# Kernel optimization log

Hardware: AMD Instinct MI355X
Metric: run time of the kernel (lower is better)

Reference implementation:

```python
import jax, jax.numpy as jnp
import numpy as np
from jax import lax

IMG = 1280
VAR0, VAR1 = 0.1, 0.2          # SSD decode variances
CONF_T = 0.7                    # confidence threshold
NMS_T = 0.4                     # IoU threshold
K = 1000                        # fixed NMS candidate budget (jit-friendly)
MIN_SIZES = [[16, 32], [64, 128], [256, 512]]
STEPS = [8, 16, 32]


def make_priors():
    """Vectorized priorbox: [cx, cy, w, h] normalized to [0,1]. N = 67200."""
    out = []
    for ms, s in zip(MIN_SIZES, STEPS):
        f = IMG // s
        ii, jj = np.meshgrid(np.arange(f), np.arange(f), indexing='ij')
        cx = (jj + 0.5) * s / IMG
        cy = (ii + 0.5) * s / IMG
        per_m = [np.stack([cx, cy, np.full_like(cx, m / IMG, dtype=np.float64),
                           np.full_like(cx, m / IMG, dtype=np.float64)], axis=-1)
                 for m in ms]
        a = np.stack(per_m, axis=2)  # [f, f, n_min_sizes, 4] -> matches (i, j, min_size) loop order
        out.append(a.reshape(-1, 4))
    return np.concatenate(out, axis=0).astype(np.float32)


def setup_inputs() -> dict:
    key = jax.random.key(0)
    k1, k2, k3 = jax.random.split(key, 3)
    N = 67200
    loc = jax.random.normal(k1, (1, N, 4), dtype=jnp.float32)
    conf = jax.random.normal(k2, (1, N, 2), dtype=jnp.float32)
    land = jax.random.normal(k3, (1, N, 10), dtype=jnp.float32)
    priors = jnp.asarray(make_priors())
    return {"loc": loc, "conf": conf, "land": land, "priors": priors}


def _decode_boxes(loc, priors):
    # center-form decode then convert to corner form (x1,y1,x2,y2)
    xy = priors[:, :2] + loc[:, :2] * VAR0 * priors[:, 2:]
    wh = priors[:, 2:] * jnp.exp(loc[:, 2:] * VAR1)
    x1y1 = xy - wh * 0.5
    return jnp.concatenate([x1y1, x1y1 + wh], axis=-1)


def _decode_landm(land, priors):
    l = land.reshape(-1, 5, 2)  # 5 landmark points
    pts = priors[:, None, :2] + l * VAR0 * priors[:, None, 2:]
    return pts.reshape(-1, 10)


def _pairwise_iou(b):
    # b: [K, 4] corner-form
    area = (b[:, 2] - b[:, 0]) * (b[:, 3] - b[:, 1])
    lt = jnp.maximum(b[:, None, :2], b[None, :, :2])
    rb = jnp.minimum(b[:, None, 2:], b[None, :, 2:])
    wh = jnp.clip(rb - lt, 0.0)
    inter = wh[..., 0] * wh[..., 1]
    return inter / (area[:, None] + area[None, :] - inter + 1e-12)


def reference(loc, conf, land, priors):
    scores_all = jax.nn.softmax(conf[0], axis=-1)[:, 1]          # [N]
    boxes_all = _decode_boxes(loc[0], priors) * IMG              # [N, 4]
    landms_all = _decode_landm(land[0], priors) * IMG            # [N, 10]

    # threshold (torch.where) + fixed-size top-K selection for jit
    masked = jnp.where(scores_all > CONF_T, scores_all, -jnp.inf)
    top_s, idx = lax.top_k(masked, K)                            # sorted descending
    b = boxes_all[idx]
    lm = landms_all[idx]
    s = scores_all[idx]
    valid = top_s > CONF_T                                       # slots that passed threshold

    # greedy NMS over score-sorted candidates
    iou = _pairwise_iou(b)                                       # [K, K]
    ar = jnp.arange(K)

    def body(i, keep):
        sup = (iou[i] > NMS_T) & (ar > i) & keep[i]
        return keep & ~sup

    keep = lax.fori_loop(0, K, body, valid)

    boxes_out = jnp.where(keep[:, None], b, 0.0)
    scores_out = jnp.where(keep, s, 0.0)
    landms_out = jnp.where(keep[:, None], lm, 0.0)
    return boxes_out, scores_out, landms_out
```

## Files before the change

### kernel.cpp

```cpp
#include <hip/hip_runtime.h>
#include <stdint.h>

#define N_ANCH 67200
#define KCAP   1000
#define CONF_THR 0.7f
#define NMS_THR  0.4f

#define BUCK_BASE 0x3F333333u
#define BUCK_SHIFT 10
#define NBUCK 5120
#define CAPG 4096

#define MID_BLKS 32
#define SUP_BLKS 63

#define OFF_CTR   0
#define OFF_HIST  64
#define OFF_FILL  20544
#define OFF_LIST  41024
#define OFF_GKEYS 578624
#define OFF_SCORE 611392
#define OFF_BOX   615488
#define OFF_LM    631872
#define OFF_SUP   672832

__device__ inline unsigned long long shfl_xor_u64(unsigned long long v, int m) {
    unsigned int lo = (unsigned int)__shfl_xor((int)(v & 0xffffffffull), m, 64);
    unsigned int hi = (unsigned int)__shfl_xor((int)(v >> 32), m, 64);
    return ((unsigned long long)hi << 32) | lo;
}

__device__ inline int bucket_of(unsigned int sb) {
    return min((int)((sb - BUCK_BASE) >> BUCK_SHIFT), NBUCK - 1);
}

__device__ inline void findcut_and_scan(int* sufx, int* swsum, int* sB,
                                        int tid, int lane, int wv) {
    if (tid < 64) {
        int acc = 0, B = 0;
        bool found = false;
        for (int t = 0; t < NBUCK / 64 && !found; ++t) {
            int base = NBUCK - 64 * (t + 1);
            int c = sufx[base + lane];
            int ssum = c;
#pragma unroll
            for (int off = 1; off < 64; off <<= 1)
                ssum += __shfl_xor(ssum, off, 64);
            if (acc + ssum >= KCAP) {
                for (int l = 63; l >= 0; --l) {
                    int cl = (int)__builtin_amdgcn_readlane((unsigned int)c, l);
                    if (acc + cl >= KCAP) { B = base + l; found = true; break; }
                    acc += cl;
                }
            } else {
                acc += ssum;
            }
        }
        if (lane == 0) *sB = found ? B : 0;
    }
    __syncthreads();
    int c[5];
#pragma unroll
    for (int k = 0; k < 5; ++k)
        c[k] = sufx[NBUCK - 1 - (tid * 5 + k)];
    int tsum = c[0] + c[1] + c[2] + c[3] + c[4];
    int inc = tsum;
#pragma unroll
    for (int off = 1; off < 64; off <<= 1) {
        int n = __shfl_up(inc, off, 64);
        if (lane >= off) inc += n;
    }
    if (lane == 63) swsum[wv] = inc;
    __syncthreads();
    if (tid < 16) {
        int v = swsum[tid];
        int s = v;
#pragma unroll
        for (int off = 1; off < 16; off <<= 1) {
            int n = __shfl_up(s, off, 64);
            if (tid >= off) s += n;
        }
        swsum[tid] = s - v;
    }
    __syncthreads();
    int run = swsum[wv] + inc - tsum;
#pragma unroll
    for (int k = 0; k < 5; ++k) {
        sufx[NBUCK - 1 - (tid * 5 + k)] = run;
        run += c[k];
    }
    __syncthreads();
}

__global__ __launch_bounds__(1024) void k_zero(int* __restrict__ ctr,
                                               int* __restrict__ hist,
                                               int* __restrict__ gfill) {
    int tid = threadIdx.x;
    if (tid < 16) ctr[tid] = 0;
    for (int t = tid; t < NBUCK; t += 1024) { hist[t] = 0; gfill[t] = 0; }
}

__global__ __launch_bounds__(256) void k_front(const float* __restrict__ conf,
                                               unsigned long long* __restrict__ list,
                                               int* __restrict__ hist,
                                               int* __restrict__ ctr) {
    int t = blockIdx.x * 256 + threadIdx.x;
    int lane = threadIdx.x & 63;
    int a0 = t * 2;
    bool p0 = false, p1 = false;
    unsigned long long k0 = 0ull, k1 = 0ull;
    if (a0 < N_ANCH) {
        float4 c = reinterpret_cast<const float4*>(conf)[t];
        {
            float mx = fmaxf(c.x, c.y);
            float e0 = expf(c.x - mx), e1 = expf(c.y - mx);
            float s = e1 / (e0 + e1);
            if (s > CONF_THR) {
                p0 = true;
                k0 = ((unsigned long long)__float_as_uint(s) << 32)
                   | (unsigned int)(0xFFFFFFFFu - (unsigned int)a0);
            }
        }
        {
            float mx = fmaxf(c.z, c.w);
            float e0 = expf(c.z - mx), e1 = expf(c.w - mx);
            float s = e1 / (e0 + e1);
            if (s > CONF_THR) {
                p1 = true;
                k1 = ((unsigned long long)__float_as_uint(s) << 32)
                   | (unsigned int)(0xFFFFFFFFu - (unsigned int)(a0 + 1));
            }
        }
    }
    unsigned long long m0 = __ballot(p0);
    unsigned long long m1 = __ballot(p1);
    int n0 = (int)__popcll(m0), n1 = (int)__popcll(m1);
    int base = 0;
    if ((n0 + n1) > 0) {
        if (lane == 0) base = atomicAdd(&ctr[0], n0 + n1);
        base = __shfl(base, 0, 64);
        unsigned long long below = (1ull << lane) - 1ull;
        if (p0) {
            list[base + (int)__popcll(m0 & below)] = k0;
            atomicAdd(&hist[bucket_of((unsigned int)(k0 >> 32))], 1);
        }
        if (p1) {
            list[base + n0 + (int)__popcll(m1 & below)] = k1;
            atomicAdd(&hist[bucket_of((unsigned int)(k1 >> 32))], 1);
        }
    }
}

__global__ __launch_bounds__(1024) void k_midrank(
        const unsigned long long* __restrict__ list,
        const int* __restrict__ hist,
        int* __restrict__ gfill,
        unsigned long long* __restrict__ gkeys,
        int* __restrict__ ctr,
        const float* __restrict__ loc,
        const float* __restrict__ land,
        const float* __restrict__ priors,
        float* __restrict__ sel_score,
        float* __restrict__ sel_box,
        float* __restrict__ sel_lm) {
#pragma clang fp contract(off)
    __shared__ int sufx[NBUCK];
    __shared__ int swsum[16];
    __shared__ int sB;
    __shared__ int slast;
    int tid = threadIdx.x, lane = tid & 63, wv = tid >> 6;
    for (int t = tid; t < NBUCK; t += 1024) sufx[t] = hist[t];
    __syncthreads();
    findcut_and_scan(sufx, swsum, &sB, tid, lane, wv);
    int B = sB;
    int M = min(ctr[0], N_ANCH);

    for (int p = blockIdx.x * 1024 + tid; p < M; p += MID_BLKS * 1024) {
        unsigned long long k = list[p];
        int b = bucket_of((unsigned int)(k >> 32));
        if (b >= B) {
            int off = atomicAdd(&gfill[b], 1);
            int slot = sufx[b] + off;
            if (slot < CAPG) gkeys[slot] = k;
        }
    }
    __syncthreads();
    if (tid == 0) {
        __threadfence();
        int old = atomicAdd(&ctr[1], 1);
        slast = (old == MID_BLKS - 1);
    }
    __syncthreads();
    if (!slast) return;
    if (tid == 0) __threadfence();
    __syncthreads();

    int S = min((B > 0) ? sufx[B - 1] : M, CAPG);
    for (int s = tid; s < S; s += 1024) {
        unsigned long long key = gkeys[s];
        unsigned int sb = (unsigned int)(key >> 32);
        int b = bucket_of(sb);
        int seg0 = sufx[b];
        int segn = gfill[b];
        int within = 0;
        for (int t = 0; t < segn && seg0 + t < CAPG; ++t)
            within += (gkeys[seg0 + t] > key) ? 1 : 0;
        int r = seg0 + within;
        if (r < KCAP) {
            unsigned int a = 0xFFFFFFFFu - (unsigned int)(key & 0xFFFFFFFFull);
            sel_score[r] = __uint_as_float(sb);
            float pcx = priors[a*4+0], pcy = priors[a*4+1];
            float pw  = priors[a*4+2], ph  = priors[a*4+3];
            float l0 = loc[a*4+0], l1 = loc[a*4+1], l2 = loc[a*4+2], l3 = loc[a*4+3];
            float cx = pcx + (l0 * 0.1f) * pw;
            float cy = pcy + (l1 * 0.1f) * ph;
            float w  = pw * expf(l2 * 0.2f);
            float h2 = ph * expf(l3 * 0.2f);
            float x1 = cx - w * 0.5f;
            float y1 = cy - h2 * 0.5f;
            sel_box[r*4+0] = x1 * 1280.0f;
            sel_box[r*4+1] = y1 * 1280.0f;
            sel_box[r*4+2] = (x1 + w) * 1280.0f;
            sel_box[r*4+3] = (y1 + h2) * 1280.0f;
#pragma unroll
            for (int q = 0; q < 5; ++q) {
                float lx = land[a*10 + 2*q + 0];
                float ly = land[a*10 + 2*q + 1];
                sel_lm[r*10 + 2*q + 0] = (pcx + (lx * 0.1f) * pw) * 1280.0f;
                sel_lm[r*10 + 2*q + 1] = (pcy + (ly * 0.1f) * ph) * 1280.0f;
            }
        }
    }
}

__global__ __launch_bounds__(1024) void k_supscan(
        const float* __restrict__ sel_box,
        const float* __restrict__ sel_score,
        const float* __restrict__ sel_lm,
        int* __restrict__ ctr,
        unsigned long long* __restrict__ sup,
        float* __restrict__ out) {
#pragma clang fp contract(off)
    __shared__ unsigned long long sup_r[1024][16];
    __shared__ unsigned long long mshare[16];
    __shared__ unsigned long long keep_final[16];
    __shared__ int slast;
    int tid = threadIdx.x;
    int wave = tid >> 6, lane = tid & 63;
    int V = min(ctr[0], KCAP);

    {
        int i = blockIdx.x * 16 + wave;
        if (i < KCAP) {
            bool irow = (i < V);
            float ax1 = 0.f, ay1 = 0.f, ax2 = 0.f, ay2 = 0.f, aarea = 0.f;
            if (irow) {
                ax1 = sel_box[i*4+0]; ay1 = sel_box[i*4+1];
                ax2 = sel_box[i*4+2]; ay2 = sel_box[i*4+3];
                aarea = (ax2 - ax1) * (ay2 - ay1);
            }
            for (int g = 0; g < 16; ++g) {
                int j = g * 64 + lane;
                bool pred = false;
                if (irow && j < V && j > i) {
                    float4 b = reinterpret_cast<const float4*>(sel_box)[j];
                    float barea = (b.z - b.x) * (b.w - b.y);
                    float ltx = fmaxf(ax1, b.x), lty = fmaxf(ay1, b.y);
                    float rbx = fminf(ax2, b.z), rby = fminf(ay2, b.w);
                    float wx = fmaxf(rbx - ltx, 0.0f);
                    float wy = fmaxf(rby - lty, 0.0f);
                    float inter = wx * wy;
                    float iou = inter / (aarea + barea - inter + 1e-12f);
                    pred = iou > NMS_THR;
                }
                unsigned long long mask = __ballot(pred);
                if (lane == 0) sup[i*16 + g] = mask;
            }
        }
    }
    __syncthreads();
    if (tid == 0) {
        __threadfence();
        int old = atomicAdd(&ctr[2], 1);
        slast = (old == SUP_BLKS - 1);
    }
    __syncthreads();
    if (!slast) return;
    if (tid == 0) __threadfence();
    __syncthreads();

    {
        const ulonglong2* sup2 = reinterpret_cast<const ulonglong2*>(sup);
        for (int idx = tid; idx < KCAP * 8; idx += 1024) {
            ulonglong2 v = sup2[idx];
            int e0 = idx * 2;
            int r = e0 >> 4, w0 = e0 & 15;
            sup_r[r][w0 ^ (r & 15)] = v.x;
            sup_r[r][(w0 + 1) ^ (r & 15)] = v.y;
        }
    }
    if (tid < 24 * 16) {
        int r = 1000 + (tid >> 4), w = tid & 15;
        sup_r[r][w ^ (r & 15)] = 0ull;
    }
    unsigned long long kw;
    {
        int lo = wave * 64;
        kw = (V >= lo + 64) ? ~0ull : (V <= lo ? 0ull : ((1ull << (V - lo)) - 1ull));
    }
    __syncthreads();

    for (int c = 0; c < 16; ++c) {
        if (wave == c) {
            unsigned long long drow = sup_r[c*64 + lane][c ^ (lane & 15)];
            unsigned int dlo = (unsigned int)drow;
            unsigned int dhi = (unsigned int)(drow >> 32);
            unsigned long long nz = __ballot(drow != 0ull);
            unsigned long long m = kw;
            unsigned long long todo = m & nz;
            while (todo) {
                int i = (int)__builtin_ctzll(todo);
                i = __builtin_amdgcn_readfirstlane(i);
                unsigned long long di =
                    (((unsigned long long)(unsigned int)__builtin_amdgcn_readlane(dhi, i)) << 32)
                  |  (unsigned long long)(unsigned int)__builtin_amdgcn_readlane(dlo, i);
                m &= ~di;
                todo &= ~di;
                todo &= todo - 1ull;
            }
            kw = m;
            if (lane == 0) mshare[c] = m;
        }
        __syncthreads();
        if (wave > c) {
            unsigned long long m = mshare[c];
            unsigned long long contrib = ((m >> lane) & 1ull)
                ? sup_r[c*64 + lane][wave ^ (lane & 15)] : 0ull;
            if (__ballot(contrib != 0ull) != 0ull) {
#pragma unroll
                for (int off = 1; off < 64; off <<= 1)
                    contrib |= shfl_xor_u64(contrib, off);
                kw &= ~contrib;
            }
        }
    }
    if (lane == 0) keep_final[wave] = kw;
    __syncthreads();

    for (int s = tid; s < KCAP; s += 1024) {
        bool kept = ((keep_final[s >> 6] >> (s & 63)) & 1ull) != 0ull;
        float4 b = make_float4(0.f, 0.f, 0.f, 0.f);
        float sc = 0.f;
        if (kept) {
            b  = reinterpret_cast<const float4*>(sel_box)[s];
            sc = sel_score[s];
        }
        reinterpret_cast<float4*>(out)[s] = b;
        out[4000 + s] = sc;
#pragma unroll
        for (int q = 0; q < 10; ++q)
            out[5000 + s*10 + q] = kept ? sel_lm[s*10 + q] : 0.f;
    }
}

extern "C" void kernel_launch(void* const* d_in, const int* in_sizes, int n_in,
                              void* d_out, int out_size, void* d_ws, size_t ws_size,
                              hipStream_t stream) {
    const float* loc    = (const float*)d_in[0];
    const float* conf   = (const float*)d_in[1];
    const float* land   = (const float*)d_in[2];
    const float* priors = (const float*)d_in[3];
    float* out = (float*)d_out;
    char* ws = (char*)d_ws;

    int* ctr                     = (int*)(ws + OFF_CTR);
    int* hist                    = (int*)(ws + OFF_HIST);
    int* gfill                   = (int*)(ws + OFF_FILL);
    unsigned long long* list     = (unsigned long long*)(ws + OFF_LIST);
    unsigned long long* gkeys    = (unsigned long long*)(ws + OFF_GKEYS);
    float* sel_score             = (float*)(ws + OFF_SCORE);
    float* sel_box               = (float*)(ws + OFF_BOX);
    float* sel_lm                = (float*)(ws + OFF_LM);
    unsigned long long* sup      = (unsigned long long*)(ws + OFF_SUP);

    int nfb = (N_ANCH / 2 + 255) / 256;
    k_zero<<<1, 1024, 0, stream>>>(ctr, hist, gfill);
    k_front<<<nfb, 256, 0, stream>>>(conf, list, hist, ctr);
    k_midrank<<<MID_BLKS, 1024, 0, stream>>>(list, hist, gfill, gkeys, ctr,
                                             loc, land, priors,
                                             sel_score, sel_box, sel_lm);
    k_supscan<<<SUP_BLKS, 1024, 0, stream>>>(sel_box, sel_score, sel_lm, ctr,
                                             sup, out);
}
```

Before: 57.27 us.

## Drop zero kernel; use per-block segmented lists and recompute histogram in midrank

Removes the separate zeroing kernel. k_front now writes candidates into fixed per-block segments sized 512, counting them with a shared atomic and storing a per-block count, so it needs neither global atomics nor a global histogram. Each midrank block rebuilds the bucket histogram in shared memory from the segmented list and derives the total candidate count. This saves one launch and the global atomic contention, but every midrank block now scans the whole segmented list redundantly, and ctr[0] now holds V=min(M,KCAP), which may change what downstream code expects.

```diff
diff --git a/kernel.cpp b/kernel.cpp
--- a/kernel.cpp
+++ b/kernel.cpp
@@ -11,18 +11,19 @@
 #define NBUCK 5120
 #define CAPG 4096
 
+#define NFB 132
 #define MID_BLKS 32
 #define SUP_BLKS 63
 
 #define OFF_CTR   0
-#define OFF_HIST  64
-#define OFF_FILL  20544
-#define OFF_LIST  41024
-#define OFF_GKEYS 578624
-#define OFF_SCORE 611392
-#define OFF_BOX   615488
-#define OFF_LM    631872
-#define OFF_SUP   672832
+#define OFF_BCNT  64
+#define OFF_FILL  640
+#define OFF_LIST  21120
+#define OFF_GKEYS 561792
+#define OFF_SCORE 594560
+#define OFF_BOX   598656
+#define OFF_LM    615040
+#define OFF_SUP   656000
 
 __device__ inline unsigned long long shfl_xor_u64(unsigned long long v, int m) {
     unsigned int lo = (unsigned int)__shfl_xor((int)(v & 0xffffffffull), m, 64);
@@ -92,20 +93,18 @@
     __syncthreads();
 }
 
-__global__ __launch_bounds__(1024) void k_zero(int* __restrict__ ctr,
-                                               int* __restrict__ hist,
-                                               int* __restrict__ gfill) {
-    int tid = threadIdx.x;
-    if (tid < 16) ctr[tid] = 0;
-    for (int t = tid; t < NBUCK; t += 1024) { hist[t] = 0; gfill[t] = 0; }
-}
-
 __global__ __launch_bounds__(256) void k_front(const float* __restrict__ conf,
                                                unsigned long long* __restrict__ list,
-                                               int* __restrict__ hist,
+                                               int* __restrict__ bcnt,
+                                               int* __restrict__ gfill,
                                                int* __restrict__ ctr) {
-    int t = blockIdx.x * 256 + threadIdx.x;
-    int lane = threadIdx.x & 63;
+    __shared__ int lcnt;
+    int tid = threadIdx.x, lane = tid & 63;
+    int blk = blockIdx.x;
+    if (tid == 0) lcnt = 0;
+    __syncthreads();
+
+    int t = blk * 256 + tid;
     int a0 = t * 2;
     bool p0 = false, p1 = false;
     unsigned long long k0 = 0ull, k1 = 0ull;
@@ -136,24 +135,23 @@
     unsigned long long m1 = __ballot(p1);
     int n0 = (int)__popcll(m0), n1 = (int)__popcll(m1);
     int base = 0;
-    if ((n0 + n1) > 0) {
-        if (lane == 0) base = atomicAdd(&ctr[0], n0 + n1);
-        base = __shfl(base, 0, 64);
-        unsigned long long below = (1ull << lane) - 1ull;
-        if (p0) {
-            list[base + (int)__popcll(m0 & below)] = k0;
-            atomicAdd(&hist[bucket_of((unsigned int)(k0 >> 32))], 1);
-        }
-        if (p1) {
-            list[base + n0 + (int)__popcll(m1 & below)] = k1;
-            atomicAdd(&hist[bucket_of((unsigned int)(k1 >> 32))], 1);
-        }
+    if (lane == 0 && (n0 + n1) > 0) base = atomicAdd(&lcnt, n0 + n1);
+    base = __shfl(base, 0, 64);
+    unsigned long long below = (1ull << lane) - 1ull;
+    int gbase = blk * 512;
+    if (p0) list[gbase + base + (int)__popcll(m0 & below)] = k0;
+    if (p1) list[gbase + base + n0 + (int)__popcll(m1 & below)] = k1;
+    __syncthreads();
+    if (tid == 0) bcnt[blk] = lcnt;
+    if (blk == 0) {
+        for (int i = tid; i < NBUCK; i += 256) gfill[i] = 0;
+        if (tid == 0) { ctr[1] = 0; ctr[2] = 0; }
     }
 }
 
 __global__ __launch_bounds__(1024) void k_midrank(
         const unsigned long long* __restrict__ list,
-        const int* __restrict__ hist,
+        const int* __restrict__ bcnt,
         int* __restrict__ gfill,
         unsigned long long* __restrict__ gkeys,
         int* __restrict__ ctr,
@@ -164,24 +162,55 @@
         float* __restrict__ sel_box,
         float* __restrict__ sel_lm) {
 #pragma clang fp contract(off)
+    __shared__ int scnt[NFB];
     __shared__ int sufx[NBUCK];
     __shared__ int swsum[16];
-    __shared__ int sB;
+    __shared__ int sB, sM;
     __shared__ int slast;
     int tid = threadIdx.x, lane = tid & 63, wv = tid >> 6;
-    for (int t = tid; t < NBUCK; t += 1024) sufx[t] = hist[t];
-    __syncthreads();
+    int bid = blockIdx.x;
+
+    if (tid < NFB) scnt[tid] = bcnt[tid];
+    for (int t = tid; t < NBUCK; t += 1024) sufx[t] = 0;
+    __syncthreads();
+
+    if (tid < 64) {
+        int v = 0;
+#pragma unroll
+        for (int c = 0; c < 3; ++c) {
+            int idx = c * 64 + lane;
+            if (idx < NFB) v += scnt[idx];
+        }
+#pragma unroll
+        for (int off = 1; off < 64; off <<= 1) v += __shfl_xor(v, off, 64);
+        if (lane == 0) sM = v;
+    }
+
+    for (int slot = tid; slot < NFB * 512; slot += 1024) {
+        int seg = slot >> 9, off = slot & 511;
+        if (off < scnt[seg]) {
+            unsigned long long k = list[slot];
+            atomicAdd(&sufx[bucket_of((unsigned int)(k >> 32))], 1);
+        }
+    }
+    __syncthreads();
+
     findcut_and_scan(sufx, swsum, &sB, tid, lane, wv);
     int B = sB;
-    int M = min(ctr[0], N_ANCH);
-
-    for (int p = blockIdx.x * 1024 + tid; p < M; p += MID_BLKS * 1024) {
-        unsigned long long k = list[p];
-        int b = bucket_of((unsigned int)(k >> 32));
-        if (b >= B) {
-            int off = atomicAdd(&gfill[b], 1);
-            int slot = sufx[b] + off;
-            if (slot < CAPG) gkeys[slot] = k;
+    int M = sM;
+    int V = min(M, KCAP);
+    if (tid == 0) ctr[0] = V;
+
+    for (int slot = bid * 1024 + tid; slot < NFB * 512; slot += MID_BLKS * 1024) {
+        int seg = slot >> 9, off = slot & 511;
+        if (off < scnt[seg]) {
+            unsigned long long k = list[slot];
+            int b = bucket_of((unsigned int)(k >> 32));
+            if (b >= B) {
+                int o = atomicAdd(&gfill[b], 1);
+                int pos = sufx[b] + o;
+                if (pos < CAPG) gkeys[pos] = k;
+            }
         }
     }
     __syncthreads();
@@ -374,7 +403,7 @@
     char* ws = (char*)d_ws;
 
     int* ctr                     = (int*)(ws + OFF_CTR);
-    int* hist                    = (int*)(ws + OFF_HIST);
+    int* bcnt                    = (int*)(ws + OFF_BCNT);
     int* gfill                   = (int*)(ws + OFF_FILL);
     unsigned long long* list     = (unsigned long long*)(ws + OFF_LIST);
     unsigned long long* gkeys    = (unsigned long long*)(ws + OFF_GKEYS);
@@ -383,10 +412,8 @@
     float* sel_lm                = (float*)(ws + OFF_LM);
     unsigned long long* sup      = (unsigned long long*)(ws + OFF_SUP);
 
-    int nfb = (N_ANCH / 2 + 255) / 256;
-    k_zero<<<1, 1024, 0, stream>>>(ctr, hist, gfill);
-    k_front<<<nfb, 256, 0, stream>>>(conf, list, hist, ctr);
-    k_midrank<<<MID_BLKS, 1024, 0, stream>>>(list, hist, gfill, gkeys, ctr,
+    k_front<<<NFB, 256, 0, stream>>>(conf, list, bcnt, gfill, ctr);
+    k_midrank<<<MID_BLKS, 1024, 0, stream>>>(list, bcnt, gfill, gkeys, ctr,
                                              loc, land, priors,
                                              sel_score, sel_box, sel_lm);
     k_supscan<<<SUP_BLKS, 1024, 0, stream>>>(sel_box, sel_score, sel_lm, ctr,
```

After: 69.42 us. +21.2%, slower.
